# Performance work log

Hardware: AMD Instinct MI355X
Metric: run time of the kernel (lower is better)

## Reference

```python
import jax, jax.numpy as jnp
import numpy as np

N = 100000
E = 1600000
IN_F = 128
H_F = 128


def _sage_layer(h, weights, src, dst, W_self, b_self, W_neigh):
    # message: w_e * h[src]  -> [E, F]
    m = h[src] * weights[:, None]
    # segment-mean over destination nodes (DGL fn.mean divides by in-degree)
    s = jax.ops.segment_sum(m, dst, num_segments=N)
    deg = jax.ops.segment_sum(jnp.ones((E,), h.dtype), dst, num_segments=N)
    neigh = s / jnp.maximum(deg, 1.0)[:, None]
    # DGL SAGEConv('mean'): fc_self(h) + fc_neigh(neigh); bias lives in fc_self
    return h @ W_self.T + b_self + neigh @ W_neigh.T


def setup_inputs() -> dict:
    key = jax.random.key(0)
    ks = jax.random.split(key, 10)
    scale_in = 1.0 / np.sqrt(IN_F)
    scale_h = 1.0 / np.sqrt(H_F)
    return {
        "in_feat": jax.random.normal(ks[0], (N, IN_F), jnp.float32),
        "weights": jax.random.uniform(ks[1], (E,), jnp.float32),
        "src": jax.random.randint(ks[2], (E,), 0, N),
        "dst": jax.random.randint(ks[3], (E,), 0, N),
        "W_self1": jax.random.normal(ks[4], (H_F, IN_F), jnp.float32) * scale_in,
        "b_self1": jnp.zeros((H_F,), jnp.float32),
        "W_neigh1": jax.random.normal(ks[5], (H_F, IN_F), jnp.float32) * scale_in,
        "W_self2": jax.random.normal(ks[6], (H_F, H_F), jnp.float32) * scale_h,
        "b_self2": jnp.zeros((H_F,), jnp.float32),
        "W_neigh2": jax.random.normal(ks[7], (H_F, H_F), jnp.float32) * scale_h,
    }


def reference(in_feat, weights, src, dst, W_self1, b_self1, W_neigh1, W_self2, b_self2, W_neigh2):
    h = _sage_layer(in_feat, weights, src, dst, W_self1, b_self1, W_neigh1)
    h = jax.nn.relu(h)
    h = _sage_layer(h, weights, src, dst, W_self2, b_self2, W_neigh2)
    return h
```

## Files before the change

kernel.cpp:

```cpp
#include <hip/hip_runtime.h>


#define NN 100000
#define NE 1600000
#define F 128

#define SCAN_BS 1024
#define NBLK ((NN + SCAN_BS - 1) / SCAN_BS)

#define NPB 128
#define NPB_BITS 7
#define NBUK ((NN + NPB - 1) / NPB)
#define EPB 4096
#define NBLK3 ((NE + EPB - 1) / EPB)

static const size_t CNT_OFF   = 0;
static const size_t ROW_OFF   = 400000;
static const size_t BSUM_OFF  = 800016;
static const size_t EDGE_OFF  = 804112;
static const size_t WCAT1_OFF = 13604112;
static const size_t WCAT2_OFF = 13669648;
static const size_t SBF_OFF   = 13735184;
static const size_t H1BF_OFF  = 39335184;
static const size_t WS_NEED   = 64935184;

static const size_t FB_S_OFF = 524288;

typedef __attribute__((ext_vector_type(8))) short short8;
typedef __attribute__((ext_vector_type(4))) float float4v;

__device__ __forceinline__ float bf2f(unsigned int u16) {
    unsigned int x = u16 << 16;
    float f;
    __builtin_memcpy(&f, &x, 4);
    return f;
}
__device__ __forceinline__ unsigned int f2bf(float f) {
    unsigned int x;
    __builtin_memcpy(&x, &f, 4);
    unsigned int r = x + 0x7FFFu + ((x >> 16) & 1u);
    return r >> 16;
}

__device__ __forceinline__ void gload_lds16(const unsigned short* g, unsigned short* l) {
    __builtin_amdgcn_global_load_lds(
        (const __attribute__((address_space(1))) unsigned int*)(g),
        (__attribute__((address_space(3))) unsigned int*)(l), 16, 0, 0);
}


__global__ __launch_bounds__(256) void count_kernel(const int* __restrict__ dst,
                                                    int* __restrict__ cnt) {
    int e = blockIdx.x * 256 + threadIdx.x;
    if (e < NE) atomicAdd(&cnt[dst[e]], 1);
}

__global__ __launch_bounds__(256) void scan1_kernel(const int* __restrict__ cnt,
                                                    int* __restrict__ part,
                                                    int* __restrict__ bsum) {
    __shared__ int ts[256];
    int t = threadIdx.x;
    int base = blockIdx.x * SCAN_BS + t * 4;
    int c0 = (base     < NN) ? cnt[base]     : 0;
    int c1 = (base + 1 < NN) ? cnt[base + 1] : 0;
    int c2 = (base + 2 < NN) ? cnt[base + 2] : 0;
    int c3 = (base + 3 < NN) ? cnt[base + 3] : 0;
    int sum = c0 + c1 + c2 + c3;
    ts[t] = sum;
    __syncthreads();
    for (int off = 1; off < 256; off <<= 1) {
        int u = (t >= off) ? ts[t - off] : 0;
        __syncthreads();
        ts[t] += u;
        __syncthreads();
    }
    int excl = ts[t] - sum;
    if (t == 255) bsum[blockIdx.x] = ts[255];
    if (base     < NN) part[base]     = excl;
    if (base + 1 < NN) part[base + 1] = excl + c0;
    if (base + 2 < NN) part[base + 2] = excl + c0 + c1;
    if (base + 3 < NN) part[base + 3] = excl + c0 + c1 + c2;
}

__global__ __launch_bounds__(128) void scan2_kernel(int* __restrict__ bsum) {
    __shared__ int ts[128];
    int t = threadIdx.x;
    int v = (t < NBLK) ? bsum[t] : 0;
    ts[t] = v;
    __syncthreads();
    for (int off = 1; off < 128; off <<= 1) {
        int u = (t >= off) ? ts[t - off] : 0;
        __syncthreads();
        ts[t] += u;
        __syncthreads();
    }
    if (t < NBLK) bsum[t] = ts[t] - v;
}

__global__ __launch_bounds__(256) void scan3_kernel(int* __restrict__ part,
                                                    const int* __restrict__ bsum,
                                                    int* __restrict__ bcur) {
    int i = blockIdx.x * 256 + threadIdx.x;
    if (i < NN) {
        int v = part[i] + bsum[i / SCAN_BS];
        part[i] = v;
        if ((i & (NPB - 1)) == 0) bcur[i >> NPB_BITS] = v;
    }
    if (i == 0) part[NN] = NE;
}


__global__ __launch_bounds__(256) void bscatter(const int* __restrict__ src,
                                                const int* __restrict__ dst,
                                                const float* __restrict__ w,
                                                int* __restrict__ bcur,
                                                int2* __restrict__ ebuf) {
    __shared__ int2 rec[EPB];
    __shared__ unsigned short bid[EPB];
    __shared__ int hist[NBUK];
    __shared__ int gbase[NBUK];
    __shared__ int cur[NBUK];

    int t = threadIdx.x;
    for (int i = t; i < NBUK; i += 256) { hist[i] = 0; cur[i] = 0; }
    __syncthreads();

    int base_e = blockIdx.x * EPB;
#pragma unroll
    for (int i = 0; i < 16; i++) {
        int idx = i * 256 + t;
        int e = base_e + idx;
        if (e < NE) {
            int d = dst[e];
            int b = d >> NPB_BITS;
            int2 r;
            r.x = src[e] | ((d & (NPB - 1)) << 17);
            r.y = __float_as_int(w[e]);
            rec[idx] = r;
            bid[idx] = (unsigned short)b;
            atomicAdd(&hist[b], 1);
        } else {
            bid[idx] = 0xFFFFu;
        }
    }
    __syncthreads();

    for (int i = t; i < NBUK; i += 256)
        if (hist[i] > 0) gbase[i] = atomicAdd(&bcur[i], hist[i]);
    __syncthreads();

#pragma unroll
    for (int i = 0; i < 16; i++) {
        int idx = i * 256 + t;
        int b = bid[idx];
        if (b != 0xFFFFu) {
            int r = atomicAdd(&cur[b], 1);
            ebuf[gbase[b] + r] = rec[idx];
        }
    }
}

__global__ __launch_bounds__(256) void fine_fill(const int* __restrict__ row,
                                                 const int2* __restrict__ ebuf,
                                                 int2* __restrict__ edge) {
    __shared__ int lcur[NPB];
    int b = blockIdx.x;
    int t = threadIdx.x;
    int n0 = b * NPB;
    int n1 = min(n0 + NPB, NN);
    for (int i = t; i < n1 - n0; i += 256) lcur[i] = row[n0 + i];
    __syncthreads();
    int beg = row[n0], end = row[n1];
    for (int e = beg + t; e < end; e += 256) {
        int2 r = ebuf[e];
        int dl = (r.x >> 17) & (NPB - 1);
        int pos = atomicAdd(&lcur[dl], 1);
        int2 o;
        o.x = r.x & 0x1FFFF;
        o.y = r.y;
        edge[pos] = o;
    }
}


__global__ __launch_bounds__(256) void wprep_kernel(const float* __restrict__ Ws1,
                                                    const float* __restrict__ Wn1,
                                                    const float* __restrict__ Ws2,
                                                    const float* __restrict__ Wn2,
                                                    unsigned short* __restrict__ wcat1,
                                                    unsigned short* __restrict__ wcat2) {
    int idx = blockIdx.x * 256 + threadIdx.x;
    int which = idx >> 15;
    int j = idx & 32767;
    int n = j >> 8, k = j & 255;
    const float* Ws = which ? Ws2 : Ws1;
    const float* Wn = which ? Wn2 : Wn1;
    float v = (k < 128) ? Ws[n * 128 + k] : Wn[n * 128 + (k - 128)];
    unsigned short* o = which ? wcat2 : wcat1;
    o[j] = (unsigned short)f2bf(v);
}

__global__ __launch_bounds__(256) void conv_bf16(const float* __restrict__ in,
                                                 unsigned short* __restrict__ outbf) {
    size_t base = ((size_t)blockIdx.x * 256 + threadIdx.x) * 8;
    float4 a = *(const float4*)(in + base);
    float4 b = *(const float4*)(in + base + 4);
    uint4 p;
    p.x = f2bf(a.x) | (f2bf(a.y) << 16);
    p.y = f2bf(a.z) | (f2bf(a.w) << 16);
    p.z = f2bf(b.x) | (f2bf(b.y) << 16);
    p.w = f2bf(b.z) | (f2bf(b.w) << 16);
    *(uint4*)(outbf + base) = p;
}

__global__ __launch_bounds__(256) void gather_packed(const unsigned short* __restrict__ h,
                                                     const int* __restrict__ row,
                                                     const int2* __restrict__ edge,
                                                     unsigned short* __restrict__ sbf) {
    int t = threadIdx.x;
    int lane = t & 63;
    int n = blockIdx.x * 4 + (t >> 6);
    int beg = __builtin_amdgcn_readfirstlane(row[n]);
    int end = __builtin_amdgcn_readfirstlane(row[n + 1]);
    const unsigned int* hp = (const unsigned int*)h;

    float ax = 0.0f, ay = 0.0f;
    int e = beg;
    for (; e + 7 < end; e += 8) {
        int2 m[8];
#pragma unroll
        for (int i = 0; i < 8; i++) m[i] = edge[e + i];
        unsigned int p[8];
#pragma unroll
        for (int i = 0; i < 8; i++) p[i] = hp[(size_t)m[i].x * 64 + lane];
#pragma unroll
        for (int i = 0; i < 8; i++) {
            float wf = __int_as_float(m[i].y);
            ax += wf * bf2f(p[i] & 0xFFFFu);
            ay += wf * bf2f(p[i] >> 16);
        }
    }
    for (; e < end; e++) {
        int2 m0 = edge[e];
        unsigned int p0 = hp[(size_t)m0.x * 64 + lane];
        float wf = __int_as_float(m0.y);
        ax += wf * bf2f(p0 & 0xFFFFu);
        ay += wf * bf2f(p0 >> 16);
    }
    float invd = 1.0f / fmaxf((float)(end - beg), 1.0f);
    unsigned int outp = f2bf(ax * invd) | (f2bf(ay * invd) << 16);
    ((unsigned int*)sbf)[(size_t)n * 64 + lane] = outp;
}


__global__ __launch_bounds__(512, 4) void mfma_gemm(
    const unsigned short* self_bf,
    const unsigned short* __restrict__ sbf,
    const unsigned short* __restrict__ wcat,
    const float* __restrict__ bias,
    unsigned short* out_bf,
    float* __restrict__ out_f32)
{
    __shared__ unsigned short Bs[128][256];

    int t = threadIdx.x;
    int l = t & 63;
    int w = t >> 6;
    int base = blockIdx.x * 256;
    int lane16 = l & 15;
    int quad = l >> 4;
    int swz = (lane16 & 7) << 3;

    unsigned short* lbase = &Bs[0][0];
#pragma unroll
    for (int i = 0; i < 8; i++) {
        int idx = i * 512 + t;
        int r = idx >> 5;
        int cb = (idx & 31) << 4;
        int sb = cb ^ ((r & 7) << 4);
        gload_lds16(wcat + r * 256 + (sb >> 1), lbase + idx * 8);
    }

    int r0 = base + w * 32 + lane16;
    int r1 = r0 + 16;
    int r0c = min(r0, NN - 1);
    int r1c = min(r1, NN - 1);

    float4v acc0[8], acc1[8];
#pragma unroll
    for (int ct = 0; ct < 8; ct++) {
        acc0[ct] = (float4v){0.f, 0.f, 0.f, 0.f};
        acc1[ct] = (float4v){0.f, 0.f, 0.f, 0.f};
    }

    __syncthreads();

#pragma unroll
    for (int half = 0; half < 2; half++) {
        const unsigned short* srcb = (half == 0) ? self_bf : sbf;
        const unsigned short* p0 = srcb + (size_t)r0c * F + quad * 8;
        const unsigned short* p1 = srcb + (size_t)r1c * F + quad * 8;
        short8 Ah0[4], Ah1[4];
#pragma unroll
        for (int kk = 0; kk < 4; kk++) {
            Ah0[kk] = *(const short8*)(p0 + kk * 32);
            Ah1[kk] = *(const short8*)(p1 + kk * 32);
        }
#pragma unroll
        for (int kk = 0; kk < 4; kk++) {
#pragma unroll
            for (int ct = 0; ct < 8; ct++) {
                int r = ct * 16 + lane16;
                int col = half * 128 + kk * 32 + quad * 8;
                short8 b = *(const short8*)(lbase + (size_t)r * 256 + (col ^ swz));
                acc0[ct] = __builtin_amdgcn_mfma_f32_16x16x32_bf16(Ah0[kk], b, acc0[ct], 0, 0, 0);
                acc1[ct] = __builtin_amdgcn_mfma_f32_16x16x32_bf16(Ah1[kk], b, acc1[ct], 0, 0, 0);
            }
        }
    }

    int rowb0 = base + w * 32 + quad * 4;
    int rowb1 = rowb0 + 16;
#pragma unroll
    for (int ct = 0; ct < 8; ct++) {
        int col = ct * 16 + lane16;
        float bc = bias[col];
#pragma unroll
        for (int r = 0; r < 4; r++) {
            int g0 = rowb0 + r, g1 = rowb1 + r;
            float v0 = acc0[ct][r] + bc;
            float v1 = acc1[ct][r] + bc;
            if (out_bf) {
                v0 = fmaxf(v0, 0.0f);
                v1 = fmaxf(v1, 0.0f);
                if (g0 < NN) out_bf[(size_t)g0 * F + col] = (unsigned short)f2bf(v0);
                if (g1 < NN) out_bf[(size_t)g1 * F + col] = (unsigned short)f2bf(v1);
            } else {
                if (g0 < NN) out_f32[(size_t)g0 * F + col] = v0;
                if (g1 < NN) out_f32[(size_t)g1 * F + col] = v1;
            }
        }
    }
}


__global__ __launch_bounds__(256) void scatter_kernel(const float* __restrict__ h,
                                                      const float* __restrict__ w,
                                                      const int* __restrict__ src,
                                                      const int* __restrict__ dst,
                                                      float* __restrict__ s,
                                                      float* __restrict__ deg,
                                                      int add_deg) {
    int e = blockIdx.x * 4 + (threadIdx.x >> 6);
    int lane = threadIdx.x & 63;
    int sn = src[e];
    int dn = dst[e];
    float wf = w[e];
    float2 p = *(const float2*)(h + (size_t)sn * F + lane * 2);
    float* sp = s + (size_t)dn * F + lane * 2;
    unsafeAtomicAdd(sp,     wf * p.x);
    unsafeAtomicAdd(sp + 1, wf * p.y);
    if (add_deg && lane == 0) unsafeAtomicAdd(&deg[dn], 1.0f);
}

__global__ __launch_bounds__(256) void sage_gemm(const float* h,
                                                 const float* __restrict__ s,
                                                 const float* deg,
                                                 const float* __restrict__ Ws,
                                                 const float* __restrict__ bias,
                                                 const float* __restrict__ Wn,
                                                 float* out,
                                                 int relu) {
    __shared__ float xs[16][F];
    __shared__ float invd[16];
    int t = threadIdx.x;
    int j = t & 127;
    int g = t >> 7;
    int base = blockIdx.x * 16;
    for (int idx = t; idx < 16 * 32; idx += 256) {
        int n = idx >> 5, kq = idx & 31;
        *(float4*)&xs[n][kq * 4] = *(const float4*)(h + (size_t)(base + n) * F + kq * 4);
    }
    if (t < 16) invd[t] = deg ? 1.0f / fmaxf(deg[base + t], 1.0f) : 1.0f;
    __syncthreads();
    float acc[8];
#pragma unroll
    for (int i = 0; i < 8; i++) acc[i] = 0.0f;
    for (int kc = 0; kc < F; kc += 4) {
        float4 wv = *(const float4*)(Ws + j * F + kc);
#pragma unroll
        for (int i = 0; i < 8; i++) {
            const float* xr = &xs[g * 8 + i][kc];
            acc[i] += xr[0] * wv.x + xr[1] * wv.y + xr[2] * wv.z + xr[3] * wv.w;
        }
    }
    __syncthreads();
    for (int idx = t; idx < 16 * 32; idx += 256) {
        int n = idx >> 5, kq = idx & 31;
        float4 sv = *(const float4*)(s + (size_t)(base + n) * F + kq * 4);
        float iv = invd[n];
        xs[n][kq * 4]     = sv.x * iv;
        xs[n][kq * 4 + 1] = sv.y * iv;
        xs[n][kq * 4 + 2] = sv.z * iv;
        xs[n][kq * 4 + 3] = sv.w * iv;
    }
    __syncthreads();
    for (int kc = 0; kc < F; kc += 4) {
        float4 wv = *(const float4*)(Wn + j * F + kc);
#pragma unroll
        for (int i = 0; i < 8; i++) {
            const float* xr = &xs[g * 8 + i][kc];
            acc[i] += xr[0] * wv.x + xr[1] * wv.y + xr[2] * wv.z + xr[3] * wv.w;
        }
    }
    float bj = bias[j];
#pragma unroll
    for (int i = 0; i < 8; i++) {
        int n = base + g * 8 + i;
        float v = acc[i] + bj;
        if (relu) v = fmaxf(v, 0.0f);
        out[(size_t)n * F + j] = v;
    }
}

extern "C" void kernel_launch(void* const* d_in, const int* in_sizes, int n_in,
                              void* d_out, int out_size, void* d_ws, size_t ws_size,
                              hipStream_t stream) {
    const float* in_feat = (const float*)d_in[0];
    const float* weights = (const float*)d_in[1];
    const int* src = (const int*)d_in[2];
    const int* dst = (const int*)d_in[3];
    const float* Ws1 = (const float*)d_in[4];
    const float* b1  = (const float*)d_in[5];
    const float* Wn1 = (const float*)d_in[6];
    const float* Ws2 = (const float*)d_in[7];
    const float* b2  = (const float*)d_in[8];
    const float* Wn2 = (const float*)d_in[9];
    float* out = (float*)d_out;

    if (ws_size >= WS_NEED) {
        int* cnt    = (int*)((char*)d_ws + CNT_OFF);
        int* row    = (int*)((char*)d_ws + ROW_OFF);
        int* bsum   = (int*)((char*)d_ws + BSUM_OFF);
        int2* edge  = (int2*)((char*)d_ws + EDGE_OFF);
        unsigned short* wcat1 = (unsigned short*)((char*)d_ws + WCAT1_OFF);
        unsigned short* wcat2 = (unsigned short*)((char*)d_ws + WCAT2_OFF);
        unsigned short* sbf   = (unsigned short*)((char*)d_ws + SBF_OFF);
        int2* ebuf  = (int2*)((char*)d_ws + SBF_OFF);
        unsigned short* hbf   = (unsigned short*)((char*)d_ws + H1BF_OFF);

        hipMemsetAsync(cnt, 0, 400000, stream);
        count_kernel<<<(NE + 255) / 256, 256, 0, stream>>>(dst, cnt);
        scan1_kernel<<<NBLK, 256, 0, stream>>>(cnt, row, bsum);
        scan2_kernel<<<1, 128, 0, stream>>>(bsum);
        scan3_kernel<<<(NN + 255) / 256, 256, 0, stream>>>(row, bsum, cnt);
        bscatter<<<NBLK3, 256, 0, stream>>>(src, dst, weights, cnt, ebuf);
        fine_fill<<<NBUK, 256, 0, stream>>>(row, ebuf, edge);
        wprep_kernel<<<256, 256, 0, stream>>>(Ws1, Wn1, Ws2, Wn2, wcat1, wcat2);
        conv_bf16<<<6250, 256, 0, stream>>>(in_feat, hbf);

        gather_packed<<<NN / 4, 256, 0, stream>>>(hbf, row, edge, sbf);
        mfma_gemm<<<(NN + 255) / 256, 512, 0, stream>>>(hbf, sbf, wcat1, b1, hbf, nullptr);
        gather_packed<<<NN / 4, 256, 0, stream>>>(hbf, row, edge, sbf);
        mfma_gemm<<<(NN + 255) / 256, 512, 0, stream>>>(hbf, sbf, wcat2, b2, nullptr, out);
    } else {
        float* deg = (float*)d_ws;
        float* s   = (float*)((char*)d_ws + FB_S_OFF);
        hipMemsetAsync(d_ws, 0, FB_S_OFF + (size_t)NN * F * 4, stream);
        scatter_kernel<<<NE / 4, 256, 0, stream>>>(in_feat, weights, src, dst, s, deg, 1);
        sage_gemm<<<NN / 16, 256, 0, stream>>>(in_feat, s, deg, Ws1, b1, Wn1, out, 1);
        hipMemsetAsync(s, 0, (size_t)NN * F * 4, stream);
        scatter_kernel<<<NE / 4, 256, 0, stream>>>(out, weights, src, dst, s, deg, 0);
        sage_gemm<<<NN / 16, 256, 0, stream>>>(out, s, deg, Ws2, b2, Wn2, out, 0);
    }
}
```

Before: 428.4 us.

## Build CSR via bucket-level histogram and per-bucket local scan

Replaces the per-node global atomic degree count and three-pass node-level scan with a bucket-level LDS histogram (per 128-node bucket) and a single-block scan over buckets. Per-node row offsets are now computed inside the fine fill kernel with a local count and scan over each bucket's edges. This cuts global atomics and kernel launches in CSR construction, at the cost of reading each bucket's edges twice in the fill kernel.

```diff
diff --git a/kernel.cpp b/kernel.cpp
--- a/kernel.cpp
+++ b/kernel.cpp
@@ -4,19 +4,19 @@
 #define NN 100000
 #define NE 1600000
 #define F 128
-
-#define SCAN_BS 1024
-#define NBLK ((NN + SCAN_BS - 1) / SCAN_BS)
 
 #define NPB 128
 #define NPB_BITS 7
 #define NBUK ((NN + NPB - 1) / NPB)
 #define EPB 4096
 #define NBLK3 ((NE + EPB - 1) / EPB)
-
-static const size_t CNT_OFF   = 0;
-static const size_t ROW_OFF   = 400000;
-static const size_t BSUM_OFF  = 800016;
+#define EPB2 8192
+#define NBLK2 ((NE + EPB2 - 1) / EPB2)
+
+static const size_t BBASE_OFF = 0;
+static const size_t BCUR_OFF  = 4000;
+static const size_t BCNT_OFF  = 8000;
+static const size_t ROW_OFF   = 12000;
 static const size_t EDGE_OFF  = 804112;
 static const size_t WCAT1_OFF = 13604112;
 static const size_t WCAT2_OFF = 13669648;
@@ -49,24 +49,40 @@
 }
 
 
-__global__ __launch_bounds__(256) void count_kernel(const int* __restrict__ dst,
-                                                    int* __restrict__ cnt) {
-    int e = blockIdx.x * 256 + threadIdx.x;
-    if (e < NE) atomicAdd(&cnt[dst[e]], 1);
-}
-
-__global__ __launch_bounds__(256) void scan1_kernel(const int* __restrict__ cnt,
-                                                    int* __restrict__ part,
-                                                    int* __restrict__ bsum) {
+__global__ __launch_bounds__(256) void bcount_kernel(const int* __restrict__ dst,
+                                                     int* __restrict__ bcnt) {
+    __shared__ int hist[NBUK];
+    int t = threadIdx.x;
+    for (int i = t; i < NBUK; i += 256) hist[i] = 0;
+    __syncthreads();
+    int base_e = blockIdx.x * EPB2;
+#pragma unroll
+    for (int i = 0; i < EPB2 / 256; i++) {
+        int e = base_e + i * 256 + t;
+        if (e < NE) atomicAdd(&hist[dst[e] >> NPB_BITS], 1);
+    }
+    __syncthreads();
+    for (int i = t; i < NBUK; i += 256) {
+        int h = hist[i];
+        if (h) atomicAdd(&bcnt[i], h);
+    }
+}
+
+__global__ __launch_bounds__(256) void bscan_kernel(const int* __restrict__ bcnt,
+                                                    int* __restrict__ bbase,
+                                                    int* __restrict__ bcur) {
     __shared__ int ts[256];
     int t = threadIdx.x;
-    int base = blockIdx.x * SCAN_BS + t * 4;
-    int c0 = (base     < NN) ? cnt[base]     : 0;
-    int c1 = (base + 1 < NN) ? cnt[base + 1] : 0;
-    int c2 = (base + 2 < NN) ? cnt[base + 2] : 0;
-    int c3 = (base + 3 < NN) ? cnt[base + 3] : 0;
-    int sum = c0 + c1 + c2 + c3;
-    ts[t] = sum;
+    int v[4];
+    int base = t * 4;
+    int s = 0;
+#pragma unroll
+    for (int i = 0; i < 4; i++) {
+        int idx = base + i;
+        v[i] = (idx < NBUK) ? bcnt[idx] : 0;
+        s += v[i];
+    }
+    ts[t] = s;
     __syncthreads();
     for (int off = 1; off < 256; off <<= 1) {
         int u = (t >= off) ? ts[t - off] : 0;
@@ -74,41 +90,15 @@
         ts[t] += u;
         __syncthreads();
     }
-    int excl = ts[t] - sum;
-    if (t == 255) bsum[blockIdx.x] = ts[255];
-    if (base     < NN) part[base]     = excl;
-    if (base + 1 < NN) part[base + 1] = excl + c0;
-    if (base + 2 < NN) part[base + 2] = excl + c0 + c1;
-    if (base + 3 < NN) part[base + 3] = excl + c0 + c1 + c2;
-}
-
-__global__ __launch_bounds__(128) void scan2_kernel(int* __restrict__ bsum) {
-    __shared__ int ts[128];
-    int t = threadIdx.x;
-    int v = (t < NBLK) ? bsum[t] : 0;
-    ts[t] = v;
-    __syncthreads();
-    for (int off = 1; off < 128; off <<= 1) {
-        int u = (t >= off) ? ts[t - off] : 0;
-        __syncthreads();
-        ts[t] += u;
-        __syncthreads();
-    }
-    if (t < NBLK) bsum[t] = ts[t] - v;
-}
-
-__global__ __launch_bounds__(256) void scan3_kernel(int* __restrict__ part,
-                                                    const int* __restrict__ bsum,
-                                                    int* __restrict__ bcur) {
-    int i = blockIdx.x * 256 + threadIdx.x;
-    if (i < NN) {
-        int v = part[i] + bsum[i / SCAN_BS];
-        part[i] = v;
-        if ((i & (NPB - 1)) == 0) bcur[i >> NPB_BITS] = v;
-    }
-    if (i == 0) part[NN] = NE;
-}
-
+    int run = ts[t] - s;
+#pragma unroll
+    for (int i = 0; i < 4; i++) {
+        int idx = base + i;
+        if (idx < NBUK) { bbase[idx] = run; bcur[idx] = run; }
+        run += v[i];
+    }
+    if (t == 255) bbase[NBUK] = run;
+}
 
 __global__ __launch_bounds__(256) void bscatter(const int* __restrict__ src,
                                                 const int* __restrict__ dst,
@@ -160,17 +150,45 @@
     }
 }
 
-__global__ __launch_bounds__(256) void fine_fill(const int* __restrict__ row,
-                                                 const int2* __restrict__ ebuf,
-                                                 int2* __restrict__ edge) {
+__global__ __launch_bounds__(256) void fine_fill2(const int* __restrict__ bbase,
+                                                  const int2* __restrict__ ebuf,
+                                                  int* __restrict__ row,
+                                                  int2* __restrict__ edge) {
+    __shared__ int lcnt[NPB];
+    __shared__ int ts[NPB];
     __shared__ int lcur[NPB];
     int b = blockIdx.x;
     int t = threadIdx.x;
     int n0 = b * NPB;
-    int n1 = min(n0 + NPB, NN);
-    for (int i = t; i < n1 - n0; i += 256) lcur[i] = row[n0 + i];
-    __syncthreads();
-    int beg = row[n0], end = row[n1];
+
+    if (t < NPB) lcnt[t] = 0;
+    __syncthreads();
+
+    int beg = bbase[b], end = bbase[b + 1];
+
+    for (int e = beg + t; e < end; e += 256) {
+        int dl = (ebuf[e].x >> 17) & (NPB - 1);
+        atomicAdd(&lcnt[dl], 1);
+    }
+    __syncthreads();
+
+    int v = (t < NPB) ? lcnt[t] : 0;
+    if (t < NPB) ts[t] = v;
+    __syncthreads();
+    for (int off = 1; off < NPB; off <<= 1) {
+        int u = (t >= off && t < NPB) ? ts[t - off] : 0;
+        __syncthreads();
+        if (t < NPB) ts[t] += u;
+        __syncthreads();
+    }
+    if (t < NPB) {
+        int o = beg + ts[t] - v;
+        lcur[t] = o;
+        int n = n0 + t;
+        if (n <= NN) row[n] = o;
+    }
+    __syncthreads();
+
     for (int e = beg + t; e < end; e += 256) {
         int2 r = ebuf[e];
         int dl = (r.x >> 17) & (NPB - 1);
@@ -439,9 +457,10 @@
     float* out = (float*)d_out;
 
     if (ws_size >= WS_NEED) {
-        int* cnt    = (int*)((char*)d_ws + CNT_OFF);
+        int* bbase  = (int*)((char*)d_ws + BBASE_OFF);
+        int* bcur   = (int*)((char*)d_ws + BCUR_OFF);
+        int* bcnt   = (int*)((char*)d_ws + BCNT_OFF);
         int* row    = (int*)((char*)d_ws + ROW_OFF);
-        int* bsum   = (int*)((char*)d_ws + BSUM_OFF);
         int2* edge  = (int2*)((char*)d_ws + EDGE_OFF);
         unsigned short* wcat1 = (unsigned short*)((char*)d_ws + WCAT1_OFF);
         unsigned short* wcat2 = (unsigned short*)((char*)d_ws + WCAT2_OFF);
@@ -449,13 +468,11 @@
         int2* ebuf  = (int2*)((char*)d_ws + SBF_OFF);
         unsigned short* hbf   = (unsigned short*)((char*)d_ws + H1BF_OFF);
 
-        hipMemsetAsync(cnt, 0, 400000, stream);
-        count_kernel<<<(NE + 255) / 256, 256, 0, stream>>>(dst, cnt);
-        scan1_kernel<<<NBLK, 256, 0, stream>>>(cnt, row, bsum);
-        scan2_kernel<<<1, 128, 0, stream>>>(bsum);
-        scan3_kernel<<<(NN + 255) / 256, 256, 0, stream>>>(row, bsum, cnt);
-        bscatter<<<NBLK3, 256, 0, stream>>>(src, dst, weights, cnt, ebuf);
-        fine_fill<<<NBUK, 256, 0, stream>>>(row, ebuf, edge);
+        hipMemsetAsync(bcnt, 0, NBUK * sizeof(int), stream);
+        bcount_kernel<<<NBLK2, 256, 0, stream>>>(dst, bcnt);
+        bscan_kernel<<<1, 256, 0, stream>>>(bcnt, bbase, bcur);
+        bscatter<<<NBLK3, 256, 0, stream>>>(src, dst, weights, bcur, ebuf);
+        fine_fill2<<<NBUK, 256, 0, stream>>>(bbase, ebuf, row, edge);
         wprep_kernel<<<256, 256, 0, stream>>>(Ws1, Wn1, Ws2, Wn2, wcat1, wcat2);
         conv_bf16<<<6250, 256, 0, stream>>>(in_feat, hbf);
 
```

Result: faster. 386.2 us (-9.9%).
